# Kernel optimization log

Hardware: AMD Instinct MI355X
Metric: run time of the kernel (lower is better)

Reference implementation:

```python
import jax, jax.numpy as jnp
import numpy as np

CLASS_W, MASK_W, DICE_W = 1.0, 1.0, 1.0
BIG = 1.0e6


def _hungarian_np(cost):
    """Jonker-Volgenant style shortest-augmenting-path Hungarian (same optimum as
    scipy.optimize.linear_sum_assignment). cost: [R, C] numpy. Returns (row_ind, col_ind)
    with row_ind sorted ascending."""
    C = np.asarray(cost, dtype=np.float64)
    transposed = C.shape[0] > C.shape[1]
    if transposed:
        C = C.T
    n, m = C.shape  # n <= m
    u = np.zeros(n + 1)
    v = np.zeros(m + 1)
    p = np.zeros(m + 1, dtype=np.int64)   # p[j] = row (1-based) matched to col j
    way = np.zeros(m + 1, dtype=np.int64)
    for i in range(1, n + 1):
        p[0] = i
        j0 = 0
        minv = np.full(m + 1, np.inf)
        used = np.zeros(m + 1, dtype=bool)
        while True:
            used[j0] = True
            i0 = p[j0]
            free = ~used
            free[0] = False
            js = np.nonzero(free)[0]
            cur = C[i0 - 1, js - 1] - u[i0] - v[js]
            upd = cur < minv[js]
            minv[js] = np.where(upd, cur, minv[js])
            way[js] = np.where(upd, j0, way[js])
            j1 = js[np.argmin(minv[js])]
            delta = minv[j1]
            u[p[used]] += delta
            v[used] -= delta
            minv[free] -= delta
            j0 = j1
            if p[j0] == 0:
                break
        while j0 != 0:
            j1 = way[j0]
            p[j0] = p[j1]
            j0 = j1
    cols = np.nonzero(p[1:])[0]
    rows = p[1:][cols] - 1
    if transposed:
        rows, cols = cols, rows
    order = np.argsort(rows)
    return rows[order], cols[order]


def _cost_matrix(pred_logits, pred_masks, target_masks, target_labels):
    B, N, H, W = pred_masks.shape
    T = target_labels.shape[1]
    HW = H * W
    # classification cost: -softmax(logits)[..., :-1][:, labels]
    out_prob = jax.nn.softmax(pred_logits, axis=-1)[..., :-1]          # [B, N, C]
    onehot = jax.nn.one_hot(target_labels, out_prob.shape[-1], dtype=out_prob.dtype)  # [B, T, C]
    cost_class = -jnp.einsum('bnc,btc->bnt', out_prob, onehot)
    # nearest-neighbor resize of target masks to pred mask resolution (torch F.interpolate 'nearest')
    Ht, Wt = target_masks.shape[-2:]
    ri = (jnp.arange(H) * Ht) // H
    ci = (jnp.arange(W) * Wt) // W
    tm = target_masks[:, :, ri][:, :, :, ci].reshape(B, T, HW)          # [B, T, HW]
    pm = pred_masks.reshape(B, N, HW)                                    # [B, N, HW]
    # sigmoid BCE cost (vs all-ones/all-zeros decomposition)
    cost_mask = jax.nn.softplus(pm).mean(-1)[:, :, None] - jnp.einsum('bnp,btp->bnt', pm, tm) / HW
    # dice cost
    ps = jax.nn.sigmoid(pm)
    numerator = 2.0 * jnp.einsum('bnp,btp->bnt', ps, tm)
    denominator = ps.sum(-1)[:, :, None] + tm.sum(-1)[:, None, :]
    cost_dice = 1.0 - (numerator + 1.0) / (denominator + 1.0)
    cost = CLASS_W * cost_class + MASK_W * cost_mask + DICE_W * cost_dice
    return jnp.nan_to_num(cost, nan=BIG, posinf=BIG, neginf=-BIG)       # [B, N, T]


_cost_matrix_jit = jax.jit(_cost_matrix)


def setup_inputs() -> dict:
    key = jax.random.key(0)
    k1, k2, k3, k4 = jax.random.split(key, 4)
    pred_logits = jax.random.normal(k1, (8, 100, 81), dtype=jnp.float32)
    pred_masks = jax.random.normal(k2, (8, 100, 256, 256), dtype=jnp.float32)
    target_masks = (jax.random.uniform(k3, (8, 32, 512, 512)) < 0.3).astype(jnp.float32)
    target_labels = jax.random.randint(k4, (8, 32), 0, 80)
    return {
        'pred_logits': pred_logits,
        'pred_masks': pred_masks,
        'target_masks': target_masks,
        'target_labels': target_labels,
    }


def reference(pred_logits, pred_masks, target_masks, target_labels):
    cost = _cost_matrix_jit(pred_logits, pred_masks, target_masks, target_labels)
    costs = np.asarray(cost)  # host sync, mirrors the original .cpu() round-trip
    src_list, tgt_list = [], []
    for b in range(costs.shape[0]):  # serial per-image assignment (inherent to Hungarian)
        r, c = _hungarian_np(costs[b])
        src_list.append(r)
        tgt_list.append(c)
    src = jnp.asarray(np.stack(src_list), dtype=jnp.int64)  # [B, T] query indices
    tgt = jnp.asarray(np.stack(tgt_list), dtype=jnp.int64)  # [B, T] target indices
    return (src, tgt)
```

## Files before the change

kernel.cpp:

```cpp
#include <hip/hip_runtime.h>
#include <stdint.h>


#define BATCH 8
#define NQ    100
#define NT    32
#define HWP   65536
#define NCLS  81
#define BIGV  1.0e6
#define MPAD  112
#define MTILES 7
#define KSPLIT 16
#define KC (HWP / KSPLIT)
#define KW (KC / 4)
#define NITER (KW / 64)

typedef __attribute__((ext_vector_type(8))) short short8;
typedef __attribute__((ext_vector_type(4))) float f32x4;

__device__ inline unsigned short f2bf(float f) {
    uint32_t u = __builtin_bit_cast(uint32_t, f);
    u += 0x7fffu + ((u >> 16) & 1u);
    return (unsigned short)(u >> 16);
}

__global__ __launch_bounds__(256) void pack_kernel(const float* __restrict__ tmask,
                                                   uint32_t* __restrict__ packed,
                                                   int* __restrict__ tm_counts) {
    int idx = blockIdx.x * 256 + threadIdx.x;
    int b = idx >> 16;
    int p = idx & 65535;
    int y = p >> 8, x = p & 255;
    const float* base = tmask + (size_t)b * NT * 262144 + (size_t)(2 * y) * 512 + (2 * x);
    uint32_t w = 0;
#pragma unroll
    for (int t = 0; t < NT; ++t) {
        float v = base[(size_t)t * 262144];
        w |= (v > 0.5f ? 1u : 0u) << t;
    }
    packed[idx] = w;
    int lane = threadIdx.x & 63;
    int mycnt = 0;
#pragma unroll
    for (int t = 0; t < NT; ++t) {
        unsigned long long m = __ballot((w >> t) & 1u);
        if (lane == t) mycnt = __popcll(m);
    }
    if (lane < NT) atomicAdd(&tm_counts[b * NT + lane], mycnt);
}

__global__ __launch_bounds__(256) void mfma_kernel(const float* __restrict__ pmask,
                                                   const uint32_t* __restrict__ packed,
                                                   float* __restrict__ accd,
                                                   float* __restrict__ accs) {
    const int kblk = blockIdx.x;
    const int mt   = blockIdx.y;
    const int b    = blockIdx.z;
    const int tid  = threadIdx.x;
    const int wv   = tid >> 6, lane = tid & 63;
    const int m0   = mt * 16;
    const int q    = lane >> 4;
    const int r    = lane & 15;

    __shared__ float Cred[8][16][32];

    int mrow = m0 + r; if (mrow > NQ - 1) mrow = NQ - 1;
    const float* Arow = pmask + (size_t)b * NQ * HWP + (size_t)mrow * HWP;
    const uint32_t* pkb = packed + (size_t)b * HWP;
    const int kbase0 = kblk * KC + wv * KW;

    f32x4 Cpm0 = {0,0,0,0}, Cpm1 = {0,0,0,0}, Csg0 = {0,0,0,0}, Csg1 = {0,0,0,0};
    float rsp = 0.f, rsg = 0.f;

    for (int ki = 0; ki < NITER; ++ki) {
        const int kb = kbase0 + ki * 64;
        const float4 va0 = *(const float4*)(Arow + kb + q * 8);
        const float4 va1 = *(const float4*)(Arow + kb + q * 8 + 4);
        const float4 va2 = *(const float4*)(Arow + kb + 32 + q * 8);
        const float4 va3 = *(const float4*)(Arow + kb + 32 + q * 8 + 4);
        const uint4  wb0 = *(const uint4*)(pkb + kb + q * 8);
        const uint4  wb1 = *(const uint4*)(pkb + kb + q * 8 + 4);
        const uint4  wb2 = *(const uint4*)(pkb + kb + 32 + q * 8);
        const uint4  wb3 = *(const uint4*)(pkb + kb + 32 + q * 8 + 4);

        short8 a0, a1, g0, g1;
        auto cvt4 = [&](const float4& v, short8& af, short8& gf, int base) {
#pragma unroll
            for (int e = 0; e < 4; ++e) {
                float pv = (&v.x)[e];
                float ax = fabsf(pv);
                float en = __expf(-ax);
                float inv = __builtin_amdgcn_rcpf(1.0f + en);
                float sig = (pv >= 0.f) ? inv : en * inv;
                float sp  = fmaxf(pv, 0.f) + __logf(1.0f + en);
                rsp += sp; rsg += sig;
                af[base + e] = (short)f2bf(pv);
                gf[base + e] = (short)f2bf(sig);
            }
        };
        cvt4(va0, a0, g0, 0); cvt4(va1, a0, g0, 4);
        cvt4(va2, a1, g1, 0); cvt4(va3, a1, g1, 4);

        short8 b00, b01, b10, b11;
        const unsigned short ONE = 0x3F80;
#pragma unroll
        for (int j = 0; j < 4; ++j) {
            uint32_t s;
            s = (&wb0.x)[j] >> r;
            b00[j]     = (short)((s & 1u)         ? ONE : 0);
            b10[j]     = (short)(((s >> 16) & 1u) ? ONE : 0);
            s = (&wb1.x)[j] >> r;
            b00[4 + j] = (short)((s & 1u)         ? ONE : 0);
            b10[4 + j] = (short)(((s >> 16) & 1u) ? ONE : 0);
            s = (&wb2.x)[j] >> r;
            b01[j]     = (short)((s & 1u)         ? ONE : 0);
            b11[j]     = (short)(((s >> 16) & 1u) ? ONE : 0);
            s = (&wb3.x)[j] >> r;
            b01[4 + j] = (short)((s & 1u)         ? ONE : 0);
            b11[4 + j] = (short)(((s >> 16) & 1u) ? ONE : 0);
        }

        Cpm0 = __builtin_amdgcn_mfma_f32_16x16x32_bf16(a0, b00, Cpm0, 0, 0, 0);
        Cpm0 = __builtin_amdgcn_mfma_f32_16x16x32_bf16(a1, b01, Cpm0, 0, 0, 0);
        Cpm1 = __builtin_amdgcn_mfma_f32_16x16x32_bf16(a0, b10, Cpm1, 0, 0, 0);
        Cpm1 = __builtin_amdgcn_mfma_f32_16x16x32_bf16(a1, b11, Cpm1, 0, 0, 0);
        Csg0 = __builtin_amdgcn_mfma_f32_16x16x32_bf16(g0, b00, Csg0, 0, 0, 0);
        Csg0 = __builtin_amdgcn_mfma_f32_16x16x32_bf16(g1, b01, Csg0, 0, 0, 0);
        Csg1 = __builtin_amdgcn_mfma_f32_16x16x32_bf16(g0, b10, Csg1, 0, 0, 0);
        Csg1 = __builtin_amdgcn_mfma_f32_16x16x32_bf16(g1, b11, Csg1, 0, 0, 0);
    }

    rsp += __shfl_xor(rsp, 16, 64);
    rsp += __shfl_xor(rsp, 32, 64);
    rsg += __shfl_xor(rsg, 16, 64);
    rsg += __shfl_xor(rsg, 32, 64);
    if (q == 0 && m0 + r < NQ) {
        atomicAdd(&accs[(size_t)b * MPAD + m0 + r], rsp);
        atomicAdd(&accs[(size_t)(BATCH + b) * MPAD + m0 + r], rsg);
    }

#pragma unroll
    for (int e = 0; e < 4; ++e) {
        const int m = q * 4 + e;
        Cred[wv * 2 + 0][m][r]      = Cpm0[e];
        Cred[wv * 2 + 0][m][16 + r] = Cpm1[e];
        Cred[wv * 2 + 1][m][r]      = Csg0[e];
        Cred[wv * 2 + 1][m][16 + r] = Csg1[e];
    }
    __syncthreads();
    for (int idx = tid; idx < 1024; idx += 256) {
        const int type = idx >> 9, rem = idx & 511, m = rem >> 5, n = rem & 31;
        float s = Cred[0 + type][m][n] + Cred[2 + type][m][n]
                + Cred[4 + type][m][n] + Cred[6 + type][m][n];
        const int gm = m0 + m;
        if (gm < NQ)
            atomicAdd(&accd[(size_t)(type * BATCH + b) * MPAD * 32 + (size_t)gm * 32 + n], s);
    }
}

__global__ __launch_bounds__(64) void hungarian_kernel(const float* __restrict__ logits,
                                                       const int* __restrict__ labels,
                                                       const float* __restrict__ accd,
                                                       const float* __restrict__ accs,
                                                       const int* __restrict__ tm_counts,
                                                       int* __restrict__ out) {
    const int b = blockIdx.x;
    const int lane = threadIdx.x;

    __shared__ double Ct[NT][NQ];
    __shared__ double u[NT + 1];
    __shared__ float smx[NQ], ssm[NQ];
    __shared__ float tcs[NT];
    __shared__ int lab[NT];

    if (lane < NT) { tcs[lane] = (float)tm_counts[b * NT + lane]; lab[lane] = labels[b * NT + lane]; }
    for (int n = lane; n < NQ; n += 64) {
        const float* lg = logits + (size_t)(b * NQ + n) * NCLS;
        float mx = -1e30f;
        for (int c = 0; c < NCLS; ++c) mx = fmaxf(mx, lg[c]);
        float s = 0.f;
        for (int c = 0; c < NCLS; ++c) s += __expf(lg[c] - mx);
        smx[n] = mx; ssm[n] = s;
    }
    if (lane <= NT) u[lane] = 0.0;
    __syncthreads();
    for (int idx = lane; idx < NQ * NT; idx += 64) {
        const int t2 = idx & 31, q2 = idx >> 5;
        float dpm = accd[(size_t)b * MPAD * 32 + q2 * 32 + t2];
        float dsg = accd[(size_t)(BATCH + b) * MPAD * 32 + q2 * 32 + t2];
        float ssp = accs[(size_t)b * MPAD + q2];
        float ssg = accs[(size_t)(BATCH + b) * MPAD + q2];
        float lg = logits[(size_t)(b * NQ + q2) * NCLS + lab[t2]];
        float prob = __expf(lg - smx[q2]) / ssm[q2];
        float c = -prob + (ssp - dpm) * (1.0f / (float)HWP)
                + 1.0f - (2.0f * dsg + 1.0f) / (ssg + tcs[t2] + 1.0f);
        if (isnan(c)) c = (float)BIGV;
        else if (isinf(c)) c = (c > 0.f) ? (float)BIGV : -(float)BIGV;
        Ct[t2][q2] = (double)c;
    }
    __syncthreads();

    const int c0 = lane + 1;
    const bool valid1 = (lane < NQ - 64);
    const int c1 = lane + 65;
    const int cidx1 = valid1 ? (lane + 64) : 0;

    double v0 = 0.0, v1 = 0.0;
    int p0 = 0, p1 = 0;
    double u_reg = 0.0;

    for (int i = 1; i <= NT; ++i) {
        double minv0 = 1e300, minv1 = 1e300;
        int way0 = 0, way1 = 0;
        bool used0 = false, used1 = !valid1;
        double du0 = 0.0, du1 = 0.0, dtot = 0.0;
        int j0 = 0, i0 = i;
        int jfin = 0;

        for (int guard = 0; guard < 160; ++guard) {
            double u_i0 = __shfl(u_reg, i0, 64);
            double cur0 = Ct[i0 - 1][lane] - u_i0 - v0;
            if (!used0 && cur0 < minv0) { minv0 = cur0; way0 = j0; }
            double cur1 = Ct[i0 - 1][cidx1] - u_i0 - v1;
            if (!used1 && cur1 < minv1) { minv1 = cur1; way1 = j0; }
            double bv = 1e301; int bj = 1 << 20;
            if (!used0) { bv = minv0; bj = c0; }
            if (!used1 && minv1 < bv) { bv = minv1; bj = c1; }
#pragma unroll
            for (int s = 32; s > 0; s >>= 1) {
                double ov = __shfl_down(bv, s, 64);
                int    oj = __shfl_down(bj, s, 64);
                if (ov < bv || (ov == bv && oj < bj)) { bv = ov; bj = oj; }
            }
            double delta = __shfl(bv, 0, 64);
            int j1 = __shfl(bj, 0, 64);
            dtot += delta;
            if (used0) { v0 -= delta; du0 += delta; } else { minv0 -= delta; }
            if (valid1) {
                if (used1) { v1 -= delta; du1 += delta; } else { minv1 -= delta; }
            }
            if (c0 == j1) used0 = true;
            if (valid1 && c1 == j1) used1 = true;
            int src = (j1 - 1) & 63, slot = (j1 - 1) >> 6;
            int pa = __shfl(p0, src, 64), pb = __shfl(p1, src, 64);
            int pj1 = slot ? pb : pa;
            if (pj1 == 0) { jfin = j1; break; }
            j0 = j1; i0 = pj1;
        }

        if (used0 && p0 != 0) u[p0] += du0;
        if (valid1 && used1 && p1 != 0) u[p1] += du1;
        if (lane == 0) u[i] += dtot;

        int jj = jfin;
        for (int guard = 0; guard < 160 && jj != 0; ++guard) {
            int src = (jj - 1) & 63, slot = (jj - 1) >> 6;
            int wa = __shfl(way0, src, 64), wb = __shfl(way1, src, 64);
            int jprev = slot ? wb : wa;
            int pnew;
            if (jprev == 0) pnew = i;
            else {
                int s2 = (jprev - 1) & 63, sl2 = (jprev - 1) >> 6;
                int pa = __shfl(p0, s2, 64), pb = __shfl(p1, s2, 64);
                pnew = sl2 ? pb : pa;
            }
            if (c0 == jj) p0 = pnew;
            if (valid1 && c1 == jj) p1 = pnew;
            jj = jprev;
        }
        __syncthreads();
        u_reg = (lane <= NT) ? u[lane] : 0.0;
    }

    unsigned long long m0 = __ballot(p0 != 0);
    unsigned long long m1 = __ballot(valid1 && p1 != 0);
    int base = b * NT;
    if (p0 != 0) {
        int rank = __popcll(m0 & ((1ull << lane) - 1ull));
        out[base + rank] = c0 - 1;
        out[BATCH * NT + base + rank] = p0 - 1;
    }
    if (valid1 && p1 != 0) {
        int rank = __popcll(m0) + __popcll(m1 & ((1ull << lane) - 1ull));
        out[base + rank] = c1 - 1;
        out[BATCH * NT + base + rank] = p1 - 1;
    }
}

extern "C" void kernel_launch(void* const* d_in, const int* in_sizes, int n_in,
                              void* d_out, int out_size, void* d_ws, size_t ws_size,
                              hipStream_t stream) {
    const float* logits = (const float*)d_in[0];
    const float* pmasks = (const float*)d_in[1];
    const float* tmasks = (const float*)d_in[2];
    const int*   labels = (const int*)d_in[3];

    uint8_t* ws = (uint8_t*)d_ws;
    uint32_t* packed = (uint32_t*)ws;
    uint8_t* zbase = ws + (size_t)BATCH * HWP * 4;
    int* tm_counts = (int*)zbase;
    float* accd = (float*)(zbase + 1024);
    float* accs = (float*)(zbase + 1024 + 229376);
    const size_t ztotal = 1024 + 229376 + 7168;

    int* out = (int*)d_out;

    hipMemsetAsync(zbase, 0, ztotal, stream);
    pack_kernel<<<BATCH * HWP / 256, 256, 0, stream>>>(tmasks, packed, tm_counts);
    mfma_kernel<<<dim3(KSPLIT, MTILES, BATCH), 256, 0, stream>>>(pmasks, packed, accd, accs);
    hungarian_kernel<<<BATCH, 64, 0, stream>>>(logits, labels, accd, accs, tm_counts, out);
}
```

Measured before the change: 598.6 us.

## Double-buffer cost-GEMM loads and add greedy row-minimum init to Hungarian

The mask/dice cost kernel now software-pipelines its global loads with two register buffers, so the next K-chunk is fetched while the current one is converted and fed to MFMA. The Hungarian kernel gains a greedy initialization pass that sets each row's dual to its row minimum and assigns the argmin column when it is still free. Rows matched this way skip the shortest-augmenting-path loop. The prefetch raises register pressure, and the greedy pass must keep the duals feasible so the result stays optimal.

```diff
diff --git a/kernel.cpp b/kernel.cpp
--- a/kernel.cpp
+++ b/kernel.cpp
@@ -72,17 +72,22 @@
     f32x4 Cpm0 = {0,0,0,0}, Cpm1 = {0,0,0,0}, Csg0 = {0,0,0,0}, Csg1 = {0,0,0,0};
     float rsp = 0.f, rsg = 0.f;
 
-    for (int ki = 0; ki < NITER; ++ki) {
+    float4 vaA[4], vaB[4];
+    uint4  wbA[4], wbB[4];
+
+    auto loadF = [&](int ki, float4* va, uint4* wb) {
         const int kb = kbase0 + ki * 64;
-        const float4 va0 = *(const float4*)(Arow + kb + q * 8);
-        const float4 va1 = *(const float4*)(Arow + kb + q * 8 + 4);
-        const float4 va2 = *(const float4*)(Arow + kb + 32 + q * 8);
-        const float4 va3 = *(const float4*)(Arow + kb + 32 + q * 8 + 4);
-        const uint4  wb0 = *(const uint4*)(pkb + kb + q * 8);
-        const uint4  wb1 = *(const uint4*)(pkb + kb + q * 8 + 4);
-        const uint4  wb2 = *(const uint4*)(pkb + kb + 32 + q * 8);
-        const uint4  wb3 = *(const uint4*)(pkb + kb + 32 + q * 8 + 4);
-
+        va[0] = *(const float4*)(Arow + kb + q * 8);
+        va[1] = *(const float4*)(Arow + kb + q * 8 + 4);
+        va[2] = *(const float4*)(Arow + kb + 32 + q * 8);
+        va[3] = *(const float4*)(Arow + kb + 32 + q * 8 + 4);
+        wb[0] = *(const uint4*)(pkb + kb + q * 8);
+        wb[1] = *(const uint4*)(pkb + kb + q * 8 + 4);
+        wb[2] = *(const uint4*)(pkb + kb + 32 + q * 8);
+        wb[3] = *(const uint4*)(pkb + kb + 32 + q * 8 + 4);
+    };
+
+    auto compute = [&](const float4* va, const uint4* wb) {
         short8 a0, a1, g0, g1;
         auto cvt4 = [&](const float4& v, short8& af, short8& gf, int base) {
 #pragma unroll
@@ -98,24 +103,24 @@
                 gf[base + e] = (short)f2bf(sig);
             }
         };
-        cvt4(va0, a0, g0, 0); cvt4(va1, a0, g0, 4);
-        cvt4(va2, a1, g1, 0); cvt4(va3, a1, g1, 4);
+        cvt4(va[0], a0, g0, 0); cvt4(va[1], a0, g0, 4);
+        cvt4(va[2], a1, g1, 0); cvt4(va[3], a1, g1, 4);
 
         short8 b00, b01, b10, b11;
         const unsigned short ONE = 0x3F80;
 #pragma unroll
         for (int j = 0; j < 4; ++j) {
             uint32_t s;
-            s = (&wb0.x)[j] >> r;
+            s = (&wb[0].x)[j] >> r;
             b00[j]     = (short)((s & 1u)         ? ONE : 0);
             b10[j]     = (short)(((s >> 16) & 1u) ? ONE : 0);
-            s = (&wb1.x)[j] >> r;
+            s = (&wb[1].x)[j] >> r;
             b00[4 + j] = (short)((s & 1u)         ? ONE : 0);
             b10[4 + j] = (short)(((s >> 16) & 1u) ? ONE : 0);
-            s = (&wb2.x)[j] >> r;
+            s = (&wb[2].x)[j] >> r;
             b01[j]     = (short)((s & 1u)         ? ONE : 0);
             b11[j]     = (short)(((s >> 16) & 1u) ? ONE : 0);
-            s = (&wb3.x)[j] >> r;
+            s = (&wb[3].x)[j] >> r;
             b01[4 + j] = (short)((s & 1u)         ? ONE : 0);
             b11[4 + j] = (short)(((s >> 16) & 1u) ? ONE : 0);
         }
@@ -128,6 +133,14 @@
         Csg0 = __builtin_amdgcn_mfma_f32_16x16x32_bf16(g1, b01, Csg0, 0, 0, 0);
         Csg1 = __builtin_amdgcn_mfma_f32_16x16x32_bf16(g0, b10, Csg1, 0, 0, 0);
         Csg1 = __builtin_amdgcn_mfma_f32_16x16x32_bf16(g1, b11, Csg1, 0, 0, 0);
+    };
+
+    loadF(0, vaA, wbA);
+    for (int ki = 0; ki < NITER; ki += 2) {
+        loadF(ki + 1, vaB, wbB);
+        compute(vaA, wbA);
+        if (ki + 2 < NITER) loadF(ki + 2, vaA, wbA);
+        compute(vaB, wbB);
     }
 
     rsp += __shfl_xor(rsp, 16, 64);
@@ -172,6 +185,7 @@
     __shared__ float smx[NQ], ssm[NQ];
     __shared__ float tcs[NT];
     __shared__ int lab[NT];
+    __shared__ unsigned char rowdone[NT + 1];
 
     if (lane < NT) { tcs[lane] = (float)tm_counts[b * NT + lane]; lab[lane] = labels[b * NT + lane]; }
     for (int n = lane; n < NQ; n += 64) {
@@ -207,9 +221,32 @@
 
     double v0 = 0.0, v1 = 0.0;
     int p0 = 0, p1 = 0;
-    double u_reg = 0.0;
 
     for (int i = 1; i <= NT; ++i) {
+        double bv = Ct[i - 1][lane]; int bj = c0;
+        if (valid1) { double t = Ct[i - 1][cidx1]; if (t < bv) { bv = t; bj = c1; } }
+#pragma unroll
+        for (int s = 32; s > 0; s >>= 1) {
+            double ov = __shfl_down(bv, s, 64);
+            int    oj = __shfl_down(bj, s, 64);
+            if (ov < bv || (ov == bv && oj < bj)) { bv = ov; bj = oj; }
+        }
+        double rmin = __shfl(bv, 0, 64);
+        int jmin = __shfl(bj, 0, 64);
+        int src = (jmin - 1) & 63, slot = (jmin - 1) >> 6;
+        int pa = __shfl(p0, src, 64), pb = __shfl(p1, src, 64);
+        int pj = slot ? pb : pa;
+        if (lane == 0) { u[i] = rmin; rowdone[i] = (pj == 0) ? 1 : 0; }
+        if (pj == 0) {
+            if (c0 == jmin) p0 = i;
+            if (valid1 && c1 == jmin) p1 = i;
+        }
+    }
+    __syncthreads();
+    double u_reg = (lane <= NT) ? u[lane] : 0.0;
+
+    for (int i = 1; i <= NT; ++i) {
+        if (rowdone[i]) continue;
         double minv0 = 1e300, minv1 = 1e300;
         int way0 = 0, way1 = 0;
         bool used0 = false, used1 = !valid1;
```

Measured after the change: 599.1 us. About the same (+0.1%).
